# Kernel tuning notes

Measured on AMD Instinct MI355X. Metric: run time of the kernel, lower is better.

## Reference

```python
import jax, jax.numpy as jnp
import numpy as np

B, T, C, H = 4, 2048, 1024, 16
D = C // H  # head dim = 64

def setup_inputs() -> dict:
    key = jax.random.key(0)
    k1, k2, k3 = jax.random.split(key, 3)
    x = jax.random.normal(k1, (B, T, C), dtype=jnp.float32)
    w_attn = jax.random.normal(k2, (C, 3 * C), dtype=jnp.float32) * 0.02
    b_attn = jnp.zeros((3 * C,), dtype=jnp.float32)
    w_proj = jax.random.normal(k3, (C, C), dtype=jnp.float32) * 0.02
    b_proj = jnp.zeros((C,), dtype=jnp.float32)
    return {"x": x, "w_attn": w_attn, "b_attn": b_attn, "w_proj": w_proj, "b_proj": b_proj}

def reference(x, w_attn, b_attn, w_proj, b_proj):
    Bx, Tx, Cx = x.shape
    qkv = x @ w_attn + b_attn  # [B, T, 3C]
    q, k, v = jnp.split(qkv, 3, axis=2)
    # [B, H, T, D]
    q = q.reshape(Bx, Tx, H, D).swapaxes(1, 2)
    k = k.reshape(Bx, Tx, H, D).swapaxes(1, 2)
    v = v.reshape(Bx, Tx, H, D).swapaxes(1, 2)
    scale = 1.0 / jnp.sqrt(jnp.asarray(D, dtype=x.dtype))
    att = jnp.einsum('bhqd,bhkd->bhqk', q, k) * scale  # [B, H, T, T]
    causal = jnp.tril(jnp.ones((Tx, Tx), dtype=bool))
    att = jnp.where(causal[None, None], att, -jnp.inf)
    att = jax.nn.softmax(att, axis=-1)
    y = jnp.einsum('bhqk,bhkd->bhqd', att, v)  # [B, H, T, D]
    y = y.swapaxes(1, 2).reshape(Bx, Tx, Cx)
    return y @ w_proj + b_proj
```

## Files before the change

kernel.cpp:

```cpp
#include <hip/hip_runtime.h>
#include <hip/hip_bf16.h>
#include <cstdint>

#define B_ 4
#define T_ 2048
#define C_ 1024
#define H_ 16
#define D_ 64

#define BM 128
#define BN 128
#define BK 64
#define NT (C_ / BK)

typedef __bf16 bf16x8 __attribute__((ext_vector_type(8)));
typedef float f32x4 __attribute__((ext_vector_type(4)));

static __device__ __forceinline__ unsigned short f2bf(float f) {
    unsigned int i = __float_as_uint(f);
    unsigned int r = (i + 0x7FFFu + ((i >> 16) & 1u)) >> 16;
    return (unsigned short)r;
}
static __device__ __forceinline__ float exp2_fast(float x) {
    float r;
    asm("v_exp_f32 %0, %1" : "=v"(r) : "v"(x));
    return r;
}

static __device__ __forceinline__ void gl_lds16(const unsigned short* g,
                                                unsigned short* l) {
    __builtin_amdgcn_global_load_lds(
        (const __attribute__((address_space(1))) unsigned int*)g,
        (__attribute__((address_space(3))) unsigned int*)l, 16, 0, 0);
}

__global__ __launch_bounds__(256)
void convert_f32_bf16(const float* __restrict__ in,
                      unsigned short* __restrict__ out, int n) {
    int i = (blockIdx.x * 256 + threadIdx.x) * 8;
    if (i < n) {
        float4 a = *(const float4*)(in + i);
        float4 b = *(const float4*)(in + i + 4);
        ushort4 s0 = {f2bf(a.x), f2bf(a.y), f2bf(a.z), f2bf(a.w)};
        ushort4 s1 = {f2bf(b.x), f2bf(b.y), f2bf(b.z), f2bf(b.w)};
        *(ushort4*)(out + i) = s0;
        *(ushort4*)(out + i + 4) = s1;
    }
}

__global__ void transpose_f32_bf16(const float* __restrict__ in,
                                   unsigned short* __restrict__ out,
                                   int R, int Cc) {
    __shared__ unsigned short tile[32][33];
    int c0 = blockIdx.x * 32;
    int r0 = blockIdx.y * 32;
    int tx = threadIdx.x, ty = threadIdx.y;
    #pragma unroll
    for (int i = ty; i < 32; i += 8)
        tile[i][tx] = f2bf(in[(size_t)(r0 + i) * Cc + c0 + tx]);
    __syncthreads();
    #pragma unroll
    for (int i = ty; i < 32; i += 8)
        out[(size_t)(c0 + i) * R + r0 + tx] = tile[tx][i];
}

#define GEMM128_CORE(APTR, ASTRIDE, BTPTR)                                    \
    int tid = threadIdx.x;                                                    \
    int nwg = gridDim.x * gridDim.y;                                          \
    int flat = blockIdx.y * gridDim.x + blockIdx.x;                           \
    int swz = (flat & 7) * (nwg >> 3) + (flat >> 3);                          \
    int bx = swz % gridDim.x;                                                 \
    int by = swz / gridDim.x;                                                 \
    int row0 = by * BM;                                                       \
    int col0 = bx * BN;                                                       \
    int wave = tid >> 6, lane = tid & 63;                                     \
    int wm = wave >> 1, wn = wave & 1;                                        \
    int m16 = lane & 15, quad = lane >> 4;                                    \
    int srow = tid >> 3;                                                      \
    int scs = ((tid & 7) ^ (srow & 7)) * 8;                                   \
    const unsigned short* aps = (APTR) + (size_t)(row0 + srow) * (ASTRIDE)    \
                                + scs;                                        \
    const unsigned short* bps = (BTPTR) + (size_t)(col0 + srow) * C_ + scs;   \
    f32x4 acc[4][4];                                                          \
    _Pragma("unroll")                                                         \
    for (int i = 0; i < 4; ++i)                                               \
    _Pragma("unroll")                                                         \
    for (int j = 0; j < 4; ++j)                                               \
        acc[i][j] = (f32x4){0.f, 0.f, 0.f, 0.f};                              \
    auto STAGE = [&](int t, int buf) {                                        \
        int koff = t * BK;                                                    \
        unsigned short* ad = smem + buf * 8192 + tid * 8;                     \
        unsigned short* bd = smem + 16384 + buf * 8192 + tid * 8;             \
        _Pragma("unroll")                                                     \
        for (int l = 0; l < 4; ++l) {                                         \
            gl_lds16(aps + (size_t)(l * 32) * (ASTRIDE) + koff, ad + l * 2048);\
            gl_lds16(bps + (size_t)(l * 32) * C_ + koff, bd + l * 2048);      \
        }                                                                     \
    };                                                                        \
    int rbA = wm * 64 + m16;                                                  \
    int rbB = wn * 64 + m16;                                                  \
    int pc0 = ((0 + quad) ^ (m16 & 7)) * 8;                                   \
    int pc1 = ((4 + quad) ^ (m16 & 7)) * 8;                                   \
    STAGE(0, 0);                                                              \
    asm volatile("s_waitcnt vmcnt(0)" ::: "memory");                          \
    __builtin_amdgcn_s_barrier();                                             \
    for (int t = 0; t < NT; ++t) {                                            \
        int buf = t & 1;                                                      \
        if (t + 1 < NT) STAGE(t + 1, buf ^ 1);                                \
        const unsigned short* Abuf = smem + buf * 8192;                       \
        const unsigned short* Bbuf = smem + 16384 + buf * 8192;               \
        bf16x8 a0[4], a1[4], b0[4], b1[4];                                    \
        _Pragma("unroll")                                                     \
        for (int i = 0; i < 4; ++i) {                                         \
            a0[i] = *(const bf16x8*)(Abuf + (rbA + i * 16) * 64 + pc0);       \
            a1[i] = *(const bf16x8*)(Abuf + (rbA + i * 16) * 64 + pc1);       \
        }                                                                     \
        _Pragma("unroll")                                                     \
        for (int j = 0; j < 4; ++j) {                                         \
            b0[j] = *(const bf16x8*)(Bbuf + (rbB + j * 16) * 64 + pc0);       \
            b1[j] = *(const bf16x8*)(Bbuf + (rbB + j * 16) * 64 + pc1);       \
        }                                                                     \
        __builtin_amdgcn_s_setprio(1);                                        \
        _Pragma("unroll")                                                     \
        for (int i = 0; i < 4; ++i)                                           \
        _Pragma("unroll")                                                     \
        for (int j = 0; j < 4; ++j) {                                         \
            acc[i][j] = __builtin_amdgcn_mfma_f32_16x16x32_bf16(              \
                a0[i], b0[j], acc[i][j], 0, 0, 0);                            \
            acc[i][j] = __builtin_amdgcn_mfma_f32_16x16x32_bf16(              \
                a1[i], b1[j], acc[i][j], 0, 0, 0);                            \
        }                                                                     \
        __builtin_amdgcn_s_setprio(0);                                        \
        asm volatile("s_waitcnt vmcnt(0)" ::: "memory");                      \
        __builtin_amdgcn_s_barrier();                                        \
    }                                                                         \
    __syncthreads();

__global__ __launch_bounds__(256, 2)
void gemm_qkv(const unsigned short* __restrict__ A,
              const unsigned short* __restrict__ Bt,
              const float* __restrict__ bias,
              unsigned short* __restrict__ qkv,
              unsigned short* __restrict__ vt,
              int M, float qscale) {
    __shared__ __align__(16) unsigned short smem[32768];
    GEMM128_CORE(A, C_, Bt)

    float bv[4];
    #pragma unroll
    for (int j = 0; j < 4; ++j)
        bv[j] = bias[col0 + wn * 64 + j * 16 + m16];

    unsigned short* wbuf = smem + wave * 2048;
    bool isV = (col0 >= 2 * C_);
    float sc = (col0 < C_) ? qscale : 1.0f;
    int b_loc = row0 >> 11;
    int trow0 = (row0 & 2047) + wm * 64;
    int head = isV ? ((col0 - 2 * C_ + wn * 64) >> 6) : 0;
    unsigned short* vtb = vt + (size_t)((b_loc * H_ + head) * 64) * T_;

    #pragma unroll
    for (int sub = 0; sub < 4; ++sub) {
        int i0 = (sub >> 1) << 1;
        int j0 = (sub & 1) << 1;
        #pragma unroll
        for (int jj = 0; jj < 2; ++jj) {
            #pragma unroll
            for (int ii = 0; ii < 2; ++ii) {
                #pragma unroll
                for (int rr = 0; rr < 4; ++rr) {
                    int rl = ii * 16 + quad * 4 + rr;
                    int cl = jj * 16 + m16;
                    unsigned short hv =
                        f2bf((acc[i0 + ii][j0 + jj][rr] + bv[j0 + jj]) * sc);
                    if (!isV) wbuf[rl * 40 + cl] = hv;
                    else      wbuf[cl * 40 + rl] = hv;
                }
            }
        }
        __builtin_amdgcn_sched_barrier(0);
        if (!isV) {
            #pragma unroll
            for (int it = 0; it < 4; ++it) {
                int rl = it * 8 + (lane >> 3);
                int cc = (lane & 7) << 2;
                uint2 v2 = *(const uint2*)&wbuf[rl * 40 + cc];
                int rowg = row0 + wm * 64 + i0 * 16 + rl;
                int colg = col0 + wn * 64 + j0 * 16 + cc;
                *(uint2*)&qkv[(size_t)rowg * (2 * C_) + colg] = v2;
            }
        } else {
            #pragma unroll
            for (int it = 0; it < 4; ++it) {
                int dsub = it * 8 + (lane >> 3);
                int tc = (lane & 7) << 2;
                uint2 v2 = *(const uint2*)&wbuf[dsub * 40 + tc];
                int d = j0 * 16 + dsub;
                int tg = trow0 + i0 * 16 + tc;
                *(uint2*)&vtb[(size_t)d * T_ + tg] = v2;
            }
        }
        __builtin_amdgcn_sched_barrier(0);
    }
}

__global__ __launch_bounds__(256, 2)
void gemm_out(const unsigned short* __restrict__ A,
              const unsigned short* __restrict__ Bt,
              const float* __restrict__ bias,
              float* __restrict__ Cmat,
              int M) {
    const int N = C_;
    __shared__ __align__(16) unsigned short smem[32768];
    GEMM128_CORE(A, (2 * C_), Bt)

    #pragma unroll
    for (int j = 0; j < 4; ++j) {
        int col = col0 + wn * 64 + j * 16 + m16;
        float bvv = bias[col];
        #pragma unroll
        for (int i = 0; i < 4; ++i) {
            int row = row0 + wm * 64 + i * 16 + quad * 4;
            #pragma unroll
            for (int rr = 0; rr < 4; ++rr)
                Cmat[(size_t)(row + rr) * N + col] = acc[i][j][rr] + bvv;
        }
    }
}

__global__ __launch_bounds__(256)
void attn_mfma(unsigned short* __restrict__ qkv,
               const unsigned short* __restrict__ vt) {
    __shared__ __align__(16) unsigned short Ks[2][64][64];
    __shared__ __align__(16) unsigned short Vs[2][64][64];
    __shared__ __align__(16) unsigned short Pb[4][16][72];

    int bh = blockIdx.x;
    int b = bh >> 4, h = bh & 15;
    int qb = (T_ / 64 - 1) - blockIdx.y;
    int tid = threadIdx.x;
    int wave = tid >> 6;
    int lane = tid & 63;
    int m16 = lane & 15, quad = lane >> 4;

    const size_t rs = 2 * C_;
    unsigned short* base = qkv + (size_t)b * T_ * rs + h * 64;
    const unsigned short* kb0 = base + C_;
    const unsigned short* vtb = vt + (size_t)bh * 64 * T_;

    int qrow = qb * 64 + wave * 16 + m16;
    const unsigned short* qp = base + (size_t)qrow * rs;
    bf16x8 qf0 = *(const bf16x8*)(qp + quad * 8);
    bf16x8 qf1 = *(const bf16x8*)(qp + 32 + quad * 8);

    f32x4 o[4];
    #pragma unroll
    for (int dt = 0; dt < 4; ++dt) o[dt] = (f32x4){0.f, 0.f, 0.f, 0.f};
    float lrow[4] = {0.f, 0.f, 0.f, 0.f};

    int qg0 = qb * 64 + wave * 16 + quad * 4;
    int ntiles = qb + 1;

    int kkey = tid >> 3, kdc = (tid & 7) << 3;
    int kswz = (((tid & 7) ^ (kkey & 7)) << 3);
    int vd = kkey, vswz = kswz;

    int kpc0 = ((0 + quad) ^ (m16 & 7)) << 3;
    int kpc1 = ((4 + quad) ^ (m16 & 7)) << 3;

    uint4 ra  = *(const uint4*)(kb0 + (size_t)kkey * rs + kdc);
    uint4 rb  = *(const uint4*)(kb0 + (size_t)(kkey + 32) * rs + kdc);
    uint4 rva = *(const uint4*)(vtb + (size_t)vd * T_ + kdc);
    uint4 rvb = *(const uint4*)(vtb + (size_t)(vd + 32) * T_ + kdc);
    *(uint4*)&Ks[0][kkey][kswz]      = ra;
    *(uint4*)&Ks[0][kkey + 32][kswz] = rb;
    *(uint4*)&Vs[0][vd][vswz]        = rva;
    *(uint4*)&Vs[0][vd + 32][vswz]   = rvb;
    if (ntiles > 1) {
        const unsigned short* kn = kb0 + (size_t)64 * rs;
        ra  = *(const uint4*)(kn + (size_t)kkey * rs + kdc);
        rb  = *(const uint4*)(kn + (size_t)(kkey + 32) * rs + kdc);
        rva = *(const uint4*)(vtb + (size_t)vd * T_ + 64 + kdc);
        rvb = *(const uint4*)(vtb + (size_t)(vd + 32) * T_ + 64 + kdc);
    }
    __syncthreads();

    for (int kt = 0; kt < ntiles; ++kt) {
        int cur = kt & 1;

        f32x4 s[4];
        #pragma unroll
        for (int st = 0; st < 4; ++st) {
            f32x4 acc = (f32x4){0.f, 0.f, 0.f, 0.f};
            bf16x8 k0 = *(const bf16x8*)&Ks[cur][st * 16 + m16][kpc0];
            bf16x8 k1 = *(const bf16x8*)&Ks[cur][st * 16 + m16][kpc1];
            acc = __builtin_amdgcn_mfma_f32_16x16x32_bf16(qf0, k0, acc, 0, 0, 0);
            acc = __builtin_amdgcn_mfma_f32_16x16x32_bf16(qf1, k1, acc, 0, 0, 0);
            s[st] = acc;
        }

        if (kt == qb) {
            #pragma unroll
            for (int st = 0; st < 4; ++st) {
                int kg = kt * 64 + st * 16 + m16;
                #pragma unroll
                for (int r = 0; r < 4; ++r)
                    if (kg > qg0 + r) s[st][r] = -1.0e30f;
            }
        }

        #pragma unroll
        for (int st = 0; st < 4; ++st) {
            #pragma unroll
            for (int r = 0; r < 4; ++r) {
                float p = exp2_fast(s[st][r]);
                lrow[r] += p;
                Pb[wave][quad * 4 + r][st * 16 + m16] = f2bf(p);
            }
        }
        __builtin_amdgcn_sched_barrier(0);

        #pragma unroll
        for (int s2 = 0; s2 < 2; ++s2) {
            bf16x8 pa = *(const bf16x8*)&Pb[wave][m16][s2 * 32 + quad * 8];
            int vpc = ((s2 * 4 + quad) ^ (m16 & 7)) << 3;
            #pragma unroll
            for (int dt = 0; dt < 4; ++dt) {
                bf16x8 vv = *(const bf16x8*)&Vs[cur][dt * 16 + m16][vpc];
                o[dt] = __builtin_amdgcn_mfma_f32_16x16x32_bf16(pa, vv, o[dt], 0, 0, 0);
            }
        }

        if (kt + 1 < ntiles) {
            int nxt = (kt + 1) & 1;
            *(uint4*)&Ks[nxt][kkey][kswz]      = ra;
            *(uint4*)&Ks[nxt][kkey + 32][kswz] = rb;
            *(uint4*)&Vs[nxt][vd][vswz]        = rva;
            *(uint4*)&Vs[nxt][vd + 32][vswz]   = rvb;
            if (kt + 2 < ntiles) {
                const unsigned short* kn = kb0 + (size_t)((kt + 2) * 64) * rs;
                ra  = *(const uint4*)(kn + (size_t)kkey * rs + kdc);
                rb  = *(const uint4*)(kn + (size_t)(kkey + 32) * rs + kdc);
                rva = *(const uint4*)(vtb + (size_t)vd * T_ + (kt + 2) * 64 + kdc);
                rvb = *(const uint4*)(vtb + (size_t)(vd + 32) * T_ + (kt + 2) * 64 + kdc);
            }
        }
        __syncthreads();
    }

    float lf[4];
    #pragma unroll
    for (int r = 0; r < 4; ++r) lf[r] = lrow[r];
    #pragma unroll
    for (int off = 1; off <= 8; off <<= 1)
        #pragma unroll
        for (int r = 0; r < 4; ++r)
            lf[r] += __shfl_xor(lf[r], off);

    #pragma unroll
    for (int r = 0; r < 4; ++r) {
        float inv = 1.0f / lf[r];
        unsigned short* op = base + (size_t)(qg0 + r) * rs;
        #pragma unroll
        for (int dt = 0; dt < 4; ++dt)
            op[dt * 16 + m16] = f2bf(o[dt][r] * inv);
    }
}

extern "C" void kernel_launch(void* const* d_in, const int* in_sizes, int n_in,
                              void* d_out, int out_size, void* d_ws, size_t ws_size,
                              hipStream_t stream) {
    const float* x      = (const float*)d_in[0];
    const float* w_attn = (const float*)d_in[1];
    const float* b_attn = (const float*)d_in[2];
    const float* w_proj = (const float*)d_in[3];
    const float* b_proj = (const float*)d_in[4];
    float* out = (float*)d_out;

    unsigned short* ws = (unsigned short*)d_ws;
    unsigned short* xb       = ws;
    unsigned short* w_attn_t = xb + (size_t)B_ * T_ * C_;
    unsigned short* w_proj_t = w_attn_t + (size_t)3 * C_ * C_;
    unsigned short* qkv      = w_proj_t + (size_t)C_ * C_;

    const size_t fixed_hw = (size_t)B_ * T_ * C_ + 4 * (size_t)C_ * C_;
    const size_t per_b_hw = (size_t)T_ * 2 * C_ + (size_t)H_ * 64 * T_;
    int bstep = (ws_size >= (fixed_hw + (size_t)B_ * per_b_hw) * sizeof(unsigned short))
                ? B_ : 1;

    int nx = B_ * T_ * C_;
    convert_f32_bf16<<<nx / 2048, 256, 0, stream>>>(x, xb, nx);
    transpose_f32_bf16<<<dim3(3 * C_ / 32, C_ / 32), dim3(32, 8), 0, stream>>>(
        w_attn, w_attn_t, C_, 3 * C_);
    transpose_f32_bf16<<<dim3(C_ / 32, C_ / 32), dim3(32, 8), 0, stream>>>(
        w_proj, w_proj_t, C_, C_);

    const float QSCALE = 0.125f * 1.44269504088896341f;

    for (int b0 = 0; b0 < B_; b0 += bstep) {
        int M = bstep * T_;
        const unsigned short* xbb = xb + (size_t)b0 * T_ * C_;
        unsigned short* vt = qkv + (size_t)bstep * T_ * 2 * C_;

        gemm_qkv<<<dim3(3 * C_ / BN, M / BM), 256, 0, stream>>>(
            xbb, w_attn_t, b_attn, qkv, vt, M, QSCALE);

        attn_mfma<<<dim3(bstep * H_, T_ / 64), 256, 0, stream>>>(qkv, vt);

        gemm_out<<<dim3(C_ / BN, M / BM), 256, 0, stream>>>(
            qkv, w_proj_t, b_proj, out + (size_t)b0 * T_ * C_, M);
    }
}
```

Before: 258.1 us.

## Stage attention K/V tiles via direct global-to-LDS loads with MFMA priority

```diff
diff --git a/kernel.cpp b/kernel.cpp
--- a/kernel.cpp
+++ b/kernel.cpp
@@ -261,32 +261,34 @@
     int qg0 = qb * 64 + wave * 16 + quad * 4;
     int ntiles = qb + 1;
 
-    int kkey = tid >> 3, kdc = (tid & 7) << 3;
-    int kswz = (((tid & 7) ^ (kkey & 7)) << 3);
-    int vd = kkey, vswz = kswz;
+    int srow = tid >> 3;
+    int schs = ((tid & 7) ^ (srow & 7)) * 8;
+    const unsigned short* kps = kb0 + (size_t)srow * rs + schs;
+    const unsigned short* vps = vtb + (size_t)srow * T_ + schs;
+    unsigned short* kdst = &Ks[0][0][0] + wave * 512;
+    unsigned short* vdst = &Vs[0][0][0] + wave * 512;
+
+    auto STAGE = [&](int kt, int buf) {
+        const unsigned short* ks = kps + (size_t)(kt * 64) * rs;
+        const unsigned short* vs = vps + kt * 64;
+        unsigned short* kd = kdst + buf * 4096;
+        unsigned short* vd = vdst + buf * 4096;
+        gl_lds16(ks, kd);
+        gl_lds16(ks + (size_t)32 * rs, kd + 2048);
+        gl_lds16(vs, vd);
+        gl_lds16(vs + (size_t)32 * T_, vd + 2048);
+    };
 
     int kpc0 = ((0 + quad) ^ (m16 & 7)) << 3;
     int kpc1 = ((4 + quad) ^ (m16 & 7)) << 3;
 
-    uint4 ra  = *(const uint4*)(kb0 + (size_t)kkey * rs + kdc);
-    uint4 rb  = *(const uint4*)(kb0 + (size_t)(kkey + 32) * rs + kdc);
-    uint4 rva = *(const uint4*)(vtb + (size_t)vd * T_ + kdc);
-    uint4 rvb = *(const uint4*)(vtb + (size_t)(vd + 32) * T_ + kdc);
-    *(uint4*)&Ks[0][kkey][kswz]      = ra;
-    *(uint4*)&Ks[0][kkey + 32][kswz] = rb;
-    *(uint4*)&Vs[0][vd][vswz]        = rva;
-    *(uint4*)&Vs[0][vd + 32][vswz]   = rvb;
-    if (ntiles > 1) {
-        const unsigned short* kn = kb0 + (size_t)64 * rs;
-        ra  = *(const uint4*)(kn + (size_t)kkey * rs + kdc);
-        rb  = *(const uint4*)(kn + (size_t)(kkey + 32) * rs + kdc);
-        rva = *(const uint4*)(vtb + (size_t)vd * T_ + 64 + kdc);
-        rvb = *(const uint4*)(vtb + (size_t)(vd + 32) * T_ + 64 + kdc);
-    }
-    __syncthreads();
+    STAGE(0, 0);
+    asm volatile("s_waitcnt vmcnt(0)" ::: "memory");
+    __builtin_amdgcn_s_barrier();
 
     for (int kt = 0; kt < ntiles; ++kt) {
         int cur = kt & 1;
+        if (kt + 1 < ntiles) STAGE(kt + 1, cur ^ 1);
 
         f32x4 s[4];
         #pragma unroll
@@ -294,8 +296,10 @@
             f32x4 acc = (f32x4){0.f, 0.f, 0.f, 0.f};
             bf16x8 k0 = *(const bf16x8*)&Ks[cur][st * 16 + m16][kpc0];
             bf16x8 k1 = *(const bf16x8*)&Ks[cur][st * 16 + m16][kpc1];
+            __builtin_amdgcn_s_setprio(1);
             acc = __builtin_amdgcn_mfma_f32_16x16x32_bf16(qf0, k0, acc, 0, 0, 0);
             acc = __builtin_amdgcn_mfma_f32_16x16x32_bf16(qf1, k1, acc, 0, 0, 0);
+            __builtin_amdgcn_s_setprio(0);
             s[st] = acc;
         }
 
@@ -324,28 +328,17 @@
         for (int s2 = 0; s2 < 2; ++s2) {
             bf16x8 pa = *(const bf16x8*)&Pb[wave][m16][s2 * 32 + quad * 8];
             int vpc = ((s2 * 4 + quad) ^ (m16 & 7)) << 3;
+            __builtin_amdgcn_s_setprio(1);
             #pragma unroll
             for (int dt = 0; dt < 4; ++dt) {
                 bf16x8 vv = *(const bf16x8*)&Vs[cur][dt * 16 + m16][vpc];
                 o[dt] = __builtin_amdgcn_mfma_f32_16x16x32_bf16(pa, vv, o[dt], 0, 0, 0);
             }
-        }
-
-        if (kt + 1 < ntiles) {
-            int nxt = (kt + 1) & 1;
-            *(uint4*)&Ks[nxt][kkey][kswz]      = ra;
-            *(uint4*)&Ks[nxt][kkey + 32][kswz] = rb;
-            *(uint4*)&Vs[nxt][vd][vswz]        = rva;
-            *(uint4*)&Vs[nxt][vd + 32][vswz]   = rvb;
-            if (kt + 2 < ntiles) {
-                const unsigned short* kn = kb0 + (size_t)((kt + 2) * 64) * rs;
-                ra  = *(const uint4*)(kn + (size_t)kkey * rs + kdc);
-                rb  = *(const uint4*)(kn + (size_t)(kkey + 32) * rs + kdc);
-                rva = *(const uint4*)(vtb + (size_t)vd * T_ + (kt + 2) * 64 + kdc);
-                rvb = *(const uint4*)(vtb + (size_t)(vd + 32) * T_ + (kt + 2) * 64 + kdc);
-            }
-        }
-        __syncthreads();
+            __builtin_amdgcn_s_setprio(0);
+        }
+
+        asm volatile("s_waitcnt vmcnt(0)" ::: "memory");
+        __builtin_amdgcn_s_barrier();
     }
 
     float lf[4];
```

Measured after the change: 256.5 us. No clear change (-0.6%).
